# Optimization experiments

Hardware: AMD Instinct MI355X
Metric: run time of the kernel (lower is better)

Reference implementation:

```python
import jax, jax.numpy as jnp
import numpy as np

B, T, D = 2, 2048, 1024
H, DH = 16, 64  # heads, head_dim; inner_dim = H*DH = D
EPS = 1e-6


def _rmsnorm(x, g):
    # torch.nn.RMSNorm over last dim with affine weight g
    return x * jax.lax.rsqrt(jnp.mean(x * x, axis=-1, keepdims=True) + EPS) * g


def _interleaved_rope(x, cos, sin):
    # x: [B, T, D]; pairs (x0, x1) rotated: rot = [-x1, x0, -x3, x2, ...]
    b, t, d = x.shape
    x2 = x.reshape(b, t, d // 2, 2)
    rot = jnp.stack([-x2[..., 1], x2[..., 0]], axis=-1).reshape(b, t, d)
    return x * cos + rot * sin


def setup_inputs() -> dict:
    key = jax.random.key(0)
    ks = jax.random.split(key, 8)
    hidden_states = jax.random.normal(ks[0], (B, T, D), dtype=jnp.float32)
    cos = jax.random.uniform(ks[1], (1, T, D), dtype=jnp.float32)
    sin = jax.random.uniform(ks[2], (1, T, D), dtype=jnp.float32)
    s = 0.02  # init scale for weights
    wq = jax.random.normal(ks[3], (D, D), dtype=jnp.float32) * s
    wk = jax.random.normal(ks[4], (D, D), dtype=jnp.float32) * s
    wv = jax.random.normal(ks[5], (D, D), dtype=jnp.float32) * s
    wo = jax.random.normal(ks[6], (D, D), dtype=jnp.float32) * s
    bq = jnp.zeros((D,), jnp.float32)
    bk = jnp.zeros((D,), jnp.float32)
    bv = jnp.zeros((D,), jnp.float32)
    bo = jnp.zeros((D,), jnp.float32)
    gq = jnp.ones((D,), jnp.float32)
    gk = jnp.ones((D,), jnp.float32)
    return {
        'hidden_states': hidden_states, 'cos': cos, 'sin': sin,
        'wq': wq, 'bq': bq, 'wk': wk, 'bk': bk, 'wv': wv, 'bv': bv,
        'gq': gq, 'gk': gk, 'wo': wo, 'bo': bo,
    }


def reference(hidden_states, cos, sin, wq, bq, wk, bk, wv, bv, gq, gk, wo, bo):
    # QKV projections (weights stored as [in, out]) + RMSNorm(q,k) + RoPE
    q = _interleaved_rope(_rmsnorm(hidden_states @ wq + bq, gq), cos, sin)
    k = _interleaved_rope(_rmsnorm(hidden_states @ wk + bk, gk), cos, sin)
    v = hidden_states @ wv + bv

    # split heads: [B, T, D] -> [B, H, T, DH]
    def split(x):
        return x.reshape(B, T, H, DH).transpose(0, 2, 1, 3)
    q, k, v = split(q), split(k), split(v)

    scale = 1.0 / jnp.sqrt(jnp.float32(DH))
    scores = jnp.einsum('bhqd,bhkd->bhqk', q, k) * scale
    attn = jax.nn.softmax(scores, axis=-1)
    out = jnp.einsum('bhqk,bhkd->bhqd', attn, v)

    # merge heads + output projection
    out = out.transpose(0, 2, 1, 3).reshape(B, T, D)
    return out @ wo + bo
```

## Files before the change

### kernel.cpp

```cpp
#include <hip/hip_runtime.h>

typedef _Float16 f16;
typedef _Float16 f16x8 __attribute__((ext_vector_type(8)));
typedef _Float16 f16x4 __attribute__((ext_vector_type(4)));
typedef _Float16 f16x2 __attribute__((ext_vector_type(2)));
typedef float f32x4 __attribute__((ext_vector_type(4)));

#define MFMA(a, b, c) __builtin_amdgcn_mfma_f32_16x16x32_f16(a, b, c, 0, 0, 0)
#define PKRTZ(a, b) __builtin_bit_cast(f16x2, __builtin_amdgcn_cvt_pkrtz(a, b))

__device__ __forceinline__ void gload16(const void* g, void* l) {
  __builtin_amdgcn_global_load_lds((const __attribute__((address_space(1))) char*)g,
                                   (__attribute__((address_space(3))) char*)l, 16, 0, 0);
}


__global__ __launch_bounds__(256) void k_cvt_hidden(const float* __restrict__ x, f16* __restrict__ y) {
  int i = blockIdx.x * 256 + threadIdx.x;
  float4 v = ((const float4*)x)[i];
  f16x4 h; h[0] = (f16)v.x; h[1] = (f16)v.y; h[2] = (f16)v.z; h[3] = (f16)v.w;
  ((f16x4*)y)[i] = h;
}

__global__ __launch_bounds__(256) void k_cvt_w(const float* __restrict__ w0, const float* __restrict__ w1,
                                               const float* __restrict__ w2, const float* __restrict__ w3,
                                               f16* __restrict__ wt) {
  int z = blockIdx.z;
  const float* w = z == 0 ? w0 : z == 1 ? w1 : z == 2 ? w2 : w3;
  f16* dst = wt + (size_t)z * 1024 * 1024;
  __shared__ float tile[64][65];
  int t = threadIdx.x;
  int k0 = blockIdx.x * 64, n0 = blockIdx.y * 64;
  int cr = t >> 4, cc = (t & 15) * 4;
#pragma unroll
  for (int p = 0; p < 4; p++) {
    int r = cr + p * 16;
    float4 v = *(const float4*)&w[(size_t)(k0 + r) * 1024 + n0 + cc];
    tile[r][cc + 0] = v.x; tile[r][cc + 1] = v.y; tile[r][cc + 2] = v.z; tile[r][cc + 3] = v.w;
  }
  __syncthreads();
#pragma unroll
  for (int p = 0; p < 4; p++) {
    int nn = cr + p * 16;
    f16x4 h;
    h[0] = (f16)tile[cc + 0][nn]; h[1] = (f16)tile[cc + 1][nn];
    h[2] = (f16)tile[cc + 2][nn]; h[3] = (f16)tile[cc + 3][nn];
    *(f16x4*)&dst[(size_t)(n0 + nn) * 1024 + k0 + cc] = h;
  }
}

template <bool OUTF32>
__device__ __forceinline__ void gemm_core(const f16* __restrict__ A, const f16* __restrict__ W,
                                          const float* __restrict__ bias,
                                          f16* __restrict__ oh, float* __restrict__ of) {
  __shared__ f16 Al[128 * 64];
  __shared__ f16 Bl[128 * 64];
  const int t = threadIdx.x;
  const int lane = t & 63, wid = t >> 6;
  const int lr = lane & 15, lg = lane >> 4;
  const int m0 = blockIdx.x * 128, n0 = blockIdx.y * 128;
  const int wm = wid >> 1, wn = wid & 1;
  const int lrow = lane >> 3;
  const int cb = (((lane & 7) ^ lrow) << 4);

  f32x4 acc[4][4] = {};

  for (int k0 = 0; k0 < 1024; k0 += 64) {
    __syncthreads();
#pragma unroll
    for (int it = 0; it < 4; it++) {
      int rbase = it * 32 + wid * 8;
      int row = rbase + lrow;
      gload16((const char*)&A[(size_t)(m0 + row) * 1024 + k0] + cb, (char*)Al + rbase * 128);
      gload16((const char*)&W[(size_t)(n0 + row) * 1024 + k0] + cb, (char*)Bl + rbase * 128);
    }
    __syncthreads();
    f16x8 af[2][4], bf[2][4];
#pragma unroll
    for (int x = 0; x < 4; x++) {
      int ra = wm * 64 + x * 16 + lr;
      int rb = wn * 64 + x * 16 + lr;
#pragma unroll
      for (int kh = 0; kh < 2; kh++) {
        int ca = (kh * 64 + lg * 16) ^ ((lr & 7) << 4);
        af[kh][x] = *(const f16x8*)((char*)Al + ra * 128 + ca);
        bf[kh][x] = *(const f16x8*)((char*)Bl + rb * 128 + ca);
      }
    }
#pragma unroll
    for (int kh = 0; kh < 2; kh++)
#pragma unroll
      for (int mt = 0; mt < 4; mt++)
#pragma unroll
        for (int nt = 0; nt < 4; nt++)
          acc[mt][nt] = MFMA(af[kh][mt], bf[kh][nt], acc[mt][nt]);
  }
#pragma unroll
  for (int mt = 0; mt < 4; mt++) {
#pragma unroll
    for (int nt = 0; nt < 4; nt++) {
      int col = n0 + wn * 64 + nt * 16 + lr;
      float bcol = bias[col];
#pragma unroll
      for (int e = 0; e < 4; e++) {
        int row = m0 + wm * 64 + mt * 16 + lg * 4 + e;
        float val = acc[mt][nt][e] + bcol;
        if (OUTF32) of[(size_t)row * 1024 + col] = val;
        else        oh[(size_t)row * 1024 + col] = (f16)val;
      }
    }
  }
}

__global__ __launch_bounds__(256, 2) void k_gemm_qkv(const f16* __restrict__ A, const f16* __restrict__ wt,
                                                     const float* __restrict__ bq, const float* __restrict__ bk,
                                                     const float* __restrict__ bv,
                                                     f16* __restrict__ q, f16* __restrict__ k, f16* __restrict__ v) {
  int z = blockIdx.z;
  gemm_core<false>(A, wt + (size_t)z * 1024 * 1024,
                   z == 0 ? bq : z == 1 ? bk : bv,
                   z == 0 ? q : z == 1 ? k : v, nullptr);
}

__global__ __launch_bounds__(256, 2) void k_gemm_o(const f16* __restrict__ A, const f16* __restrict__ wt,
                                                   const float* __restrict__ bo, float* __restrict__ out) {
  gemm_core<true>(A, wt, bo, nullptr, out);
}

__global__ __launch_bounds__(256) void k_normrope(f16* __restrict__ qh, f16* __restrict__ kh,
                                                  const float* __restrict__ gq, const float* __restrict__ gk,
                                                  const float* __restrict__ cs, const float* __restrict__ sn) {
  int row = blockIdx.x, which = blockIdx.y;
  f16* buf = which ? kh : qh;
  const float* g = which ? gk : gq;
  int t = threadIdx.x, c4 = t * 4;
  f16x4 xv = *(const f16x4*)&buf[(size_t)row * 1024 + c4];
  float x0 = xv[0], x1 = xv[1], x2 = xv[2], x3 = xv[3];
  float ss = x0 * x0 + x1 * x1 + x2 * x2 + x3 * x3;
#pragma unroll
  for (int off = 1; off < 64; off <<= 1) ss += __shfl_xor(ss, off);
  __shared__ float red[4];
  if ((t & 63) == 0) red[t >> 6] = ss;
  __syncthreads();
  float inv = rsqrtf((red[0] + red[1] + red[2] + red[3]) * (1.0f / 1024.0f) + 1e-6f);
  int tt = row & 2047;
  float4 cv = *(const float4*)&cs[(size_t)tt * 1024 + c4];
  float4 sv = *(const float4*)&sn[(size_t)tt * 1024 + c4];
  float4 gv = *(const float4*)&g[c4];
  float y0 = x0 * inv * gv.x, y1 = x1 * inv * gv.y, y2 = x2 * inv * gv.z, y3 = x3 * inv * gv.w;
  f16x4 ov;
  ov[0] = (f16)(y0 * cv.x - y1 * sv.x);
  ov[1] = (f16)(y1 * cv.y + y0 * sv.y);
  ov[2] = (f16)(y2 * cv.z - y3 * sv.z);
  ov[3] = (f16)(y3 * cv.w + y2 * sv.w);
  *(f16x4*)&buf[(size_t)row * 1024 + c4] = ov;
}

__global__ __launch_bounds__(256) void k_vtrans(const f16* __restrict__ vh, f16* __restrict__ vt) {
  __shared__ f16 tile[64][65];
  int t = threadIdx.x;
  int t0 = blockIdx.x * 64;
  int bh = blockIdx.y;
  int b = bh >> 4, h = bh & 15;
  int rr = t >> 3, c8 = (t & 7) * 8;
#pragma unroll
  for (int p = 0; p < 2; p++) {
    int r = p * 32 + rr;
    f16x8 v = *(const f16x8*)&vh[(size_t)(b * 2048 + t0 + r) * 1024 + h * 64 + c8];
#pragma unroll
    for (int j = 0; j < 8; j++) tile[r][c8 + j] = v[j];
  }
  __syncthreads();
#pragma unroll
  for (int p = 0; p < 2; p++) {
    int dh = p * 32 + rr;
    f16x8 o;
#pragma unroll
    for (int j = 0; j < 8; j++) o[j] = tile[c8 + j][dh];
    *(f16x8*)&vt[((size_t)bh * 64 + dh) * 2048 + t0 + c8] = o;
  }
}

#define ASWZ(row) ((((row) & 3) | (((row) & 8) >> 1)) << 4)

__global__ __launch_bounds__(256, 4) void k_attn(const f16* __restrict__ qh, const f16* __restrict__ kh,
                                                 const f16* __restrict__ vt, f16* __restrict__ ao) {
  __shared__ f16 Kl[2][64 * 64];
  __shared__ f16 Vl[2][64 * 64];
  const int t = threadIdx.x;
  const int lane = t & 63, wid = t >> 6;
  const int lr = lane & 15, lg = lane >> 4;
  const int lgb = lg << 4;
  const int raw = blockIdx.y * 32 + blockIdx.x;
  const int mybh = ((raw & 7) << 2) | ((raw >> 3) & 3);
  const int myq = raw >> 5;
  const int b = mybh >> 4, h = mybh & 15;
  const int q0 = myq * 64 + wid * 16;
  const f16* Qb = qh + ((size_t)(b * 2048 + q0)) * 1024 + h * 64;
  f16x8 qf0 = *(const f16x8*)&Qb[(size_t)lr * 1024 + lg * 8];
  f16x8 qf1 = *(const f16x8*)&Qb[(size_t)lr * 1024 + 32 + lg * 8];
  const f16* Kg = kh + ((size_t)b * 2048) * 1024 + h * 64;
  const f16* Vg = vt + ((size_t)mybh) * 64 * 2048;
  const int lrow = lane >> 3;
  const int sg = (lane & 7) << 4;
  const float sc = 0.125f * 1.44269504088896340736f;
  float m = -1e30f, l = 0.f;
  f32x4 acc[4] = {};

  auto stage = [&](int kvo, int bs) {
#pragma unroll
    for (int i = 0; i < 2; i++) {
      int rbase = (i * 4 + wid) * 8;
      int row = rbase + lrow;
      int cswz = sg ^ ASWZ(row);
      gload16((const char*)(Kg + (size_t)(kvo + row) * 1024) + cswz, (char*)&Kl[bs][0] + rbase * 128);
      gload16((const char*)(Vg + (size_t)row * 2048 + kvo) + cswz, (char*)&Vl[bs][0] + rbase * 128);
    }
  };

  stage(0, 0);
  __syncthreads();
  int cur = 0;

  for (int kv0 = 0; kv0 < 2048; kv0 += 64) {
    if (kv0 + 64 < 2048) stage(kv0 + 64, cur ^ 1);
    const char* Kb = (const char*)&Kl[cur][0];
    const char* Vb = (const char*)&Vl[cur][0];

    f32x4 s[4];
#pragma unroll
    for (int ks = 0; ks < 4; ks++) {
      int key = ((lr >> 2) << 3) + (lr & 3) + ((ks & 1) << 2) + ((ks >> 1) << 5);
      int sw = ASWZ(key);
      f16x8 kf0 = *(const f16x8*)(Kb + key * 128 + (lgb ^ sw));
      f16x8 kf1 = *(const f16x8*)(Kb + key * 128 + ((64 + lgb) ^ sw));
      f32x4 z = {};
      z = MFMA(kf0, qf0, z);
      z = MFMA(kf1, qf1, z);
      s[ks] = z;
    }

    float smax = fmaxf(fmaxf(s[0][0], s[0][1]), s[0][2]);
    smax = fmaxf(fmaxf(smax, s[0][3]), s[1][0]);
    smax = fmaxf(fmaxf(smax, s[1][1]), s[1][2]);
    smax = fmaxf(fmaxf(smax, s[1][3]), s[2][0]);
    smax = fmaxf(fmaxf(smax, s[2][1]), s[2][2]);
    smax = fmaxf(fmaxf(smax, s[2][3]), s[3][0]);
    smax = fmaxf(fmaxf(smax, s[3][1]), s[3][2]);
    smax = fmaxf(smax, s[3][3]);
    smax = fmaxf(smax, __shfl_xor(smax, 16));
    smax = fmaxf(smax, __shfl_xor(smax, 32));
    float smc = smax * sc;

    if (!__all(smc - m <= 8.f)) {
      float mn = fmaxf(m, smc);
      float al = exp2f(m - mn);
      m = mn;
      float alq[4];
#pragma unroll
      for (int e = 0; e < 4; e++) alq[e] = __shfl(al, lg * 4 + e);
      l *= al;
#pragma unroll
      for (int ds = 0; ds < 4; ds++)
#pragma unroll
        for (int e = 0; e < 4; e++) acc[ds][e] *= alq[e];
    }

    float sum = 0.f;
    union { f16x8 v; f16x2 h[4]; } u[2];
#pragma unroll
    for (int ks = 0; ks < 4; ks++) {
      float p0 = exp2f(fmaf(s[ks][0], sc, -m));
      float p1 = exp2f(fmaf(s[ks][1], sc, -m));
      float p2 = exp2f(fmaf(s[ks][2], sc, -m));
      float p3 = exp2f(fmaf(s[ks][3], sc, -m));
      sum += (p0 + p1) + (p2 + p3);
      u[ks >> 1].h[(ks & 1) * 2 + 0] = PKRTZ(p0, p1);
      u[ks >> 1].h[(ks & 1) * 2 + 1] = PKRTZ(p2, p3);
    }
    sum += __shfl_xor(sum, 16);
    sum += __shfl_xor(sum, 32);
    l += sum;

#pragma unroll
    for (int ds = 0; ds < 4; ds++) {
      int vrow = ds * 16 + lr;
      int sw = ASWZ(vrow);
      f16x8 vf0 = *(const f16x8*)(Vb + vrow * 128 + (lgb ^ sw));
      f16x8 vf1 = *(const f16x8*)(Vb + vrow * 128 + ((64 + lgb) ^ sw));
      acc[ds] = MFMA(u[0].v, vf0, acc[ds]);
      acc[ds] = MFMA(u[1].v, vf1, acc[ds]);
    }

    __syncthreads();
    cur ^= 1;
  }

  float lf[4];
#pragma unroll
  for (int e = 0; e < 4; e++) lf[e] = 1.f / __shfl(l, lg * 4 + e);
#pragma unroll
  for (int e = 0; e < 4; e++) {
    size_t row = (size_t)(b * 2048 + q0 + lg * 4 + e);
#pragma unroll
    for (int ds = 0; ds < 4; ds++)
      ao[row * 1024 + h * 64 + ds * 16 + lr] = (f16)(acc[ds][e] * lf[e]);
  }
}

extern "C" void kernel_launch(void* const* d_in, const int* in_sizes, int n_in,
                              void* d_out, int out_size, void* d_ws, size_t ws_size,
                              hipStream_t stream) {
  const float* hid  = (const float*)d_in[0];
  const float* cosb = (const float*)d_in[1];
  const float* sinb = (const float*)d_in[2];
  const float* wq = (const float*)d_in[3];
  const float* bq = (const float*)d_in[4];
  const float* wk = (const float*)d_in[5];
  const float* bk = (const float*)d_in[6];
  const float* wv = (const float*)d_in[7];
  const float* bv = (const float*)d_in[8];
  const float* gq = (const float*)d_in[9];
  const float* gk = (const float*)d_in[10];
  const float* wo = (const float*)d_in[11];
  const float* bo = (const float*)d_in[12];
  float* out = (float*)d_out;

  char* ws = (char*)d_ws;
  f16* aH  = (f16*)(ws);
  f16* wt  = (f16*)(ws + ((size_t)8 << 20));
  f16* qh  = (f16*)(ws + ((size_t)16 << 20));
  f16* khb = (f16*)(ws + ((size_t)24 << 20));
  f16* vhb = (f16*)(ws + ((size_t)32 << 20));
  f16* vtb = (f16*)(ws + ((size_t)40 << 20));
  f16* ao  = (f16*)(ws + ((size_t)48 << 20));

  k_cvt_hidden<<<dim3(4096), dim3(256), 0, stream>>>(hid, aH);
  k_cvt_w<<<dim3(16, 16, 4), dim3(256), 0, stream>>>(wq, wk, wv, wo, wt);
  k_gemm_qkv<<<dim3(32, 8, 3), dim3(256), 0, stream>>>(aH, wt, bq, bk, bv, qh, khb, vhb);
  k_normrope<<<dim3(4096, 2), dim3(256), 0, stream>>>(qh, khb, gq, gk, cosb, sinb);
  k_vtrans<<<dim3(32, 32), dim3(256), 0, stream>>>(vhb, vtb);
  k_attn<<<dim3(32, 32), dim3(256), 0, stream>>>(qh, khb, vtb, ao);
  k_gemm_o<<<dim3(32, 8, 1), dim3(256), 0, stream>>>(ao, wt + (size_t)3 * 1024 * 1024, bo, out);
}
```

Baseline: 154.9 us.

## Double-buffer GEMM LDS tiles and software-pipeline QK^T ahead of softmax-PV in attention

The GEMM core gains double-buffered LDS tiles, so the next K-slice's global-to-LDS loads are issued before the current slice's MFMAs, and one barrier per iteration is dropped. The attention kernel splits K and V staging and computes QK^T for the next block before finishing softmax and PV for the current one, ping-ponging two score register sets. It also raises wave priority around MFMA sections. This aims to hide load latency and overlap matrix work with softmax, at the cost of more LDS in the GEMM and more registers in attention, which may lower occupancy.

```diff
diff --git a/kernel.cpp b/kernel.cpp
--- a/kernel.cpp
+++ b/kernel.cpp
@@ -53,8 +53,8 @@
 __device__ __forceinline__ void gemm_core(const f16* __restrict__ A, const f16* __restrict__ W,
                                           const float* __restrict__ bias,
                                           f16* __restrict__ oh, float* __restrict__ of) {
-  __shared__ f16 Al[128 * 64];
-  __shared__ f16 Bl[128 * 64];
+  __shared__ f16 Al[2][128 * 64];
+  __shared__ f16 Bl[2][128 * 64];
   const int t = threadIdx.x;
   const int lane = t & 63, wid = t >> 6;
   const int lr = lane & 15, lg = lane >> 4;
@@ -65,16 +65,21 @@
 
   f32x4 acc[4][4] = {};
 
-  for (int k0 = 0; k0 < 1024; k0 += 64) {
-    __syncthreads();
+  auto stage = [&](int k0, int bs) {
 #pragma unroll
     for (int it = 0; it < 4; it++) {
       int rbase = it * 32 + wid * 8;
       int row = rbase + lrow;
-      gload16((const char*)&A[(size_t)(m0 + row) * 1024 + k0] + cb, (char*)Al + rbase * 128);
-      gload16((const char*)&W[(size_t)(n0 + row) * 1024 + k0] + cb, (char*)Bl + rbase * 128);
-    }
-    __syncthreads();
+      gload16((const char*)&A[(size_t)(m0 + row) * 1024 + k0] + cb, (char*)&Al[bs][0] + rbase * 128);
+      gload16((const char*)&W[(size_t)(n0 + row) * 1024 + k0] + cb, (char*)&Bl[bs][0] + rbase * 128);
+    }
+  };
+
+  stage(0, 0);
+  __syncthreads();
+  int cur = 0;
+  for (int k0 = 0; k0 < 1024; k0 += 64) {
+    if (k0 + 64 < 1024) stage(k0 + 64, cur ^ 1);
     f16x8 af[2][4], bf[2][4];
 #pragma unroll
     for (int x = 0; x < 4; x++) {
@@ -83,8 +88,8 @@
 #pragma unroll
       for (int kh = 0; kh < 2; kh++) {
         int ca = (kh * 64 + lg * 16) ^ ((lr & 7) << 4);
-        af[kh][x] = *(const f16x8*)((char*)Al + ra * 128 + ca);
-        bf[kh][x] = *(const f16x8*)((char*)Bl + rb * 128 + ca);
+        af[kh][x] = *(const f16x8*)((char*)&Al[cur][0] + ra * 128 + ca);
+        bf[kh][x] = *(const f16x8*)((char*)&Bl[cur][0] + rb * 128 + ca);
       }
     }
 #pragma unroll
@@ -94,6 +99,8 @@
 #pragma unroll
         for (int nt = 0; nt < 4; nt++)
           acc[mt][nt] = MFMA(af[kh][mt], bf[kh][nt], acc[mt][nt]);
+    __syncthreads();
+    cur ^= 1;
   }
 #pragma unroll
   for (int mt = 0; mt < 4; mt++) {
@@ -207,27 +214,28 @@
   float m = -1e30f, l = 0.f;
   f32x4 acc[4] = {};
 
-  auto stage = [&](int kvo, int bs) {
+  auto stageK = [&](int kvo, int bs) {
 #pragma unroll
     for (int i = 0; i < 2; i++) {
       int rbase = (i * 4 + wid) * 8;
       int row = rbase + lrow;
       int cswz = sg ^ ASWZ(row);
       gload16((const char*)(Kg + (size_t)(kvo + row) * 1024) + cswz, (char*)&Kl[bs][0] + rbase * 128);
+    }
+  };
+  auto stageV = [&](int kvo, int bs) {
+#pragma unroll
+    for (int i = 0; i < 2; i++) {
+      int rbase = (i * 4 + wid) * 8;
+      int row = rbase + lrow;
+      int cswz = sg ^ ASWZ(row);
       gload16((const char*)(Vg + (size_t)row * 2048 + kvo) + cswz, (char*)&Vl[bs][0] + rbase * 128);
     }
   };
 
-  stage(0, 0);
-  __syncthreads();
-  int cur = 0;
-
-  for (int kv0 = 0; kv0 < 2048; kv0 += 64) {
-    if (kv0 + 64 < 2048) stage(kv0 + 64, cur ^ 1);
-    const char* Kb = (const char*)&Kl[cur][0];
-    const char* Vb = (const char*)&Vl[cur][0];
-
-    f32x4 s[4];
+  auto qkt = [&](int bs, f32x4* s) {
+    const char* Kb = (const char*)&Kl[bs][0];
+    __builtin_amdgcn_s_setprio(1);
 #pragma unroll
     for (int ks = 0; ks < 4; ks++) {
       int key = ((lr >> 2) << 3) + (lr & 3) + ((ks & 1) << 2) + ((ks >> 1) << 5);
@@ -239,7 +247,10 @@
       z = MFMA(kf1, qf1, z);
       s[ks] = z;
     }
-
+    __builtin_amdgcn_s_setprio(0);
+  };
+
+  auto finish = [&](f32x4* s, int vb) {
     float smax = fmaxf(fmaxf(s[0][0], s[0][1]), s[0][2]);
     smax = fmaxf(fmaxf(smax, s[0][3]), s[1][0]);
     smax = fmaxf(fmaxf(smax, s[1][1]), s[1][2]);
@@ -282,6 +293,8 @@
     sum += __shfl_xor(sum, 32);
     l += sum;
 
+    const char* Vb = (const char*)&Vl[vb][0];
+    __builtin_amdgcn_s_setprio(1);
 #pragma unroll
     for (int ds = 0; ds < 4; ds++) {
       int vrow = ds * 16 + lr;
@@ -291,9 +304,27 @@
       acc[ds] = MFMA(u[0].v, vf0, acc[ds]);
       acc[ds] = MFMA(u[1].v, vf1, acc[ds]);
     }
-
+    __builtin_amdgcn_s_setprio(0);
+  };
+
+  f32x4 sA[4], sB[4];
+  stageK(0, 0); stageV(0, 0);
+  __syncthreads();
+  qkt(0, sA);
+  stageK(64, 1);
+  __syncthreads();
+
+  for (int i = 0; i < 32; i += 2) {
+    qkt(1, sB);
+    if (i + 2 < 32) stageK((i + 2) * 64, 0);
+    stageV((i + 1) * 64, 1);
+    finish(sA, 0);
     __syncthreads();
-    cur ^= 1;
+    if (i + 2 < 32) qkt(0, sA);
+    if (i + 3 < 32) stageK((i + 3) * 64, 1);
+    if (i + 2 < 32) stageV((i + 2) * 64, 0);
+    finish(sB, 1);
+    __syncthreads();
   }
 
   float lf[4];
```

New measurement: 151.0 us. 1.03x faster.
